# Kernel tuning notes

Measured on AMD Instinct MI355X. Metric: run time of the kernel, lower is better.

## Reference

```python
import jax, jax.numpy as jnp
import numpy as np

N_NODES = 50000
DROP_P = 0.6


def gcn_layer(x, src, dst, W, b):
    # 0P convolution: sum features of neighbors (scatter-add over edges), then linear.
    agg = jax.ops.segment_sum(x[src], dst, num_segments=N_NODES)  # [N, F]
    return agg @ W + b


def setup_inputs() -> dict:
    key = jax.random.key(0)
    k1, k2, k3, k4, k5, k6 = jax.random.split(key, 6)
    x = jax.random.normal(k1, (N_NODES, 96), dtype=jnp.float32)
    edge_index = jax.random.randint(k2, (2, 800000), 0, N_NODES, dtype=jnp.int64)
    s1 = 1.0 / np.sqrt(96.0)
    s2 = 1.0 / np.sqrt(64.0)
    W1 = jax.random.uniform(k3, (96, 64), jnp.float32, -s1, s1)
    b1 = jax.random.uniform(k4, (64,), jnp.float32, -s1, s1)
    W2 = jax.random.uniform(k5, (64, 5), jnp.float32, -s2, s2)
    b2 = jax.random.uniform(k6, (5,), jnp.float32, -s2, s2)
    return {"x": x, "edge_index": edge_index, "W1": W1, "b1": b1, "W2": W2, "b2": b2}


def reference(x, edge_index, W1, b1, W2, b2):
    src, dst = edge_index[0], edge_index[1]
    h = gcn_layer(x, src, dst, W1, b1)          # [N, hidden]
    h = jax.nn.relu(h)
    # dropout(p=0.6), deterministic mask from a fixed key
    keep = jax.random.bernoulli(jax.random.key(1), 1.0 - DROP_P, h.shape)
    h = jnp.where(keep, h / (1.0 - DROP_P), 0.0)
    out = gcn_layer(h, src, dst, W2, b2)        # [N, num_classes]
    return out
```

## Files before the change

kernel.cpp:

```cpp
#include <hip/hip_runtime.h>

#define FIN 96
#define HID 64
#define NCLS 5
#define BSH 7
#define BNODES 128
#define MAXNB 512
#define CAPSH 12
#define G1R 64
#define SXP 100

__device__ __forceinline__ unsigned rotl32(unsigned x, int d) {
    return (x << d) | (x >> (32 - d));
}

__device__ __forceinline__ void threefry2x32(unsigned k0, unsigned k1,
                                             unsigned c0, unsigned c1,
                                             unsigned& o0, unsigned& o1) {
    unsigned ks2 = k0 ^ k1 ^ 0x1BD11BDAu;
    unsigned x0 = c0 + k0, x1 = c1 + k1;
#define RND(r) { x0 += x1; x1 = rotl32(x1, r); x1 ^= x0; }
#define G0 RND(13) RND(15) RND(26) RND(6)
#define G1 RND(17) RND(29) RND(16) RND(24)
    G0; x0 += k1;  x1 += ks2 + 1u;
    G1; x0 += ks2; x1 += k0 + 2u;
    G0; x0 += k0;  x1 += k1 + 3u;
    G1; x0 += k1;  x1 += ks2 + 4u;
    G0; x0 += ks2; x1 += k0 + 5u;
#undef G0
#undef G1
#undef RND
    o0 = x0; o1 = x1;
}

__device__ __forceinline__ float drop_mask_mul(unsigned t) {
    unsigned o0, o1;
    threefry2x32(0u, 1u, 0u, t, o0, o1);
    unsigned bits = o0 ^ o1;
    float u = __uint_as_float((bits >> 9) | 0x3f800000u) - 1.0f;
    return (u < 0.4f) ? 2.5f : 0.0f;
}

__device__ __forceinline__ unsigned short f2bf(float f) {
    unsigned u = __float_as_uint(f);
    unsigned r = 0x7fffu + ((u >> 16) & 1u);
    return (unsigned short)((u + r) >> 16);
}

__device__ __forceinline__ float bflo(unsigned u) { return __uint_as_float(u << 16); }
__device__ __forceinline__ float bfhi(unsigned u) { return __uint_as_float(u & 0xffff0000u); }

__global__ __launch_bounds__(256) void gemm1_kernel(
        const float* __restrict__ x, const float* __restrict__ W,
        unsigned short* __restrict__ t1b, int* __restrict__ bktCur, int N) {
    if (blockIdx.x == 0) {
        for (int k = threadIdx.x; k < MAXNB; k += 256) bktCur[k] = k << CAPSH;
    }
    __shared__ float sX[G1R * SXP];
    __shared__ float sW[FIN * HID];
    int row0 = blockIdx.x * G1R;
    for (int i = threadIdx.x * 4; i < FIN * HID; i += 1024)
        *(float4*)&sW[i] = *(const float4*)&W[i];
    for (int i = threadIdx.x; i < G1R * (FIN / 4); i += 256) {
        int r = i / (FIN / 4), m = i % (FIN / 4);
        int gr = row0 + r;
        float4 v = make_float4(0.f, 0.f, 0.f, 0.f);
        if (gr < N) v = *(const float4*)&x[gr * FIN + m * 4];
        *(float4*)&sX[r * SXP + m * 4] = v;
    }
    __syncthreads();
    int tc = threadIdx.x & 15;
    int tr = threadIdx.x >> 4;
    float acc[4][4] = {};
    const float* xb = &sX[tr * 4 * SXP];
    for (int k = 0; k < FIN; ++k) {
        float4 w = *(const float4*)&sW[k * HID + tc * 4];
        #pragma unroll
        for (int j = 0; j < 4; ++j) {
            float xv = xb[j * SXP + k];
            acc[j][0] += xv * w.x;
            acc[j][1] += xv * w.y;
            acc[j][2] += xv * w.z;
            acc[j][3] += xv * w.w;
        }
    }
    #pragma unroll
    for (int j = 0; j < 4; ++j) {
        int gr = row0 + tr * 4 + j;
        if (gr < N) {
            ushort4 o;
            o.x = f2bf(acc[j][0]); o.y = f2bf(acc[j][1]);
            o.z = f2bf(acc[j][2]); o.w = f2bf(acc[j][3]);
            *(ushort4*)&t1b[gr * HID + tc * 4] = o;
        }
    }
}

__global__ __launch_bounds__(1024) void bin_kernel(
        const int* __restrict__ src, const int* __restrict__ dst,
        int* __restrict__ bktCur, unsigned* __restrict__ bin, int E, int NB) {
    __shared__ int hist_s[MAXNB];
    __shared__ int base_s[MAXNB];
    __shared__ int cur_s[MAXNB];
    int e0 = blockIdx.x * 4096;
    int eb = e0 + threadIdx.x * 4;
    for (int k = threadIdx.x; k < NB; k += 1024) hist_s[k] = 0;
    __syncthreads();
    int4 s4 = make_int4(0, 0, 0, 0), d4 = make_int4(-1, -1, -1, -1);
    if (eb + 3 < E) {
        s4 = *(const int4*)&src[eb];
        d4 = *(const int4*)&dst[eb];
    } else {
        int tmp[4][2];
        for (int j = 0; j < 4; ++j) {
            tmp[j][0] = (eb + j < E) ? src[eb + j] : 0;
            tmp[j][1] = (eb + j < E) ? dst[eb + j] : -1;
        }
        s4 = make_int4(tmp[0][0], tmp[1][0], tmp[2][0], tmp[3][0]);
        d4 = make_int4(tmp[0][1], tmp[1][1], tmp[2][1], tmp[3][1]);
    }
    if (d4.x >= 0) atomicAdd(&hist_s[d4.x >> BSH], 1);
    if (d4.y >= 0) atomicAdd(&hist_s[d4.y >> BSH], 1);
    if (d4.z >= 0) atomicAdd(&hist_s[d4.z >> BSH], 1);
    if (d4.w >= 0) atomicAdd(&hist_s[d4.w >> BSH], 1);
    __syncthreads();
    for (int k = threadIdx.x; k < NB; k += 1024) {
        int c = hist_s[k];
        base_s[k] = c ? atomicAdd(&bktCur[k], c) : 0;
        cur_s[k] = 0;
    }
    __syncthreads();
    int ss[4] = {s4.x, s4.y, s4.z, s4.w};
    int dd[4] = {d4.x, d4.y, d4.z, d4.w};
    #pragma unroll
    for (int j = 0; j < 4; ++j) {
        int d = dd[j];
        if (d < 0) continue;
        int k = d >> BSH;
        int slot = base_s[k] + atomicAdd(&cur_s[k], 1);
        if (slot < ((k + 1) << CAPSH))
            bin[slot] = ((unsigned)(d & (BNODES - 1)) << 16) | (unsigned)ss[j];
    }
}

__global__ __launch_bounds__(512) void sortk_kernel(
        const int* __restrict__ bktCur, const unsigned* __restrict__ bin,
        int* __restrict__ offset, int* __restrict__ count,
        unsigned short* __restrict__ sortedSrc, int N) {
    __shared__ int cnt_s[BNODES];
    __shared__ int inc_s[BNODES];
    __shared__ int cur_s[BNODES];
    int b = blockIdx.x;
    int start = b << CAPSH;
    int end = min(bktCur[b], (b + 1) << CAPSH);
    int node0 = b << BSH;
    if (threadIdx.x < BNODES) cnt_s[threadIdx.x] = 0;
    __syncthreads();
    for (int i = start + threadIdx.x; i < end; i += 512)
        atomicAdd(&cnt_s[bin[i] >> 16], 1);
    __syncthreads();
    if (threadIdx.x < BNODES)
        inc_s[threadIdx.x] = (cnt_s[threadIdx.x] + 3) & ~3;
    __syncthreads();
    #pragma unroll
    for (int off = 1; off < BNODES; off <<= 1) {
        int v = (threadIdx.x < BNODES && threadIdx.x >= off)
                ? inc_s[threadIdx.x - off] : 0;
        __syncthreads();
        if (threadIdx.x < BNODES) inc_s[threadIdx.x] += v;
        __syncthreads();
    }
    if (threadIdx.x < BNODES) {
        int pad = (cnt_s[threadIdx.x] + 3) & ~3;
        int excl = inc_s[threadIdx.x] - pad;
        cur_s[threadIdx.x] = excl;
        int node = node0 + threadIdx.x;
        if (node < N) {
            offset[node] = start + excl;
            count[node]  = cnt_s[threadIdx.x];
        }
    }
    __syncthreads();
    for (int i = start + threadIdx.x; i < end; i += 512) {
        unsigned rec = bin[i];
        int ld = (int)(rec >> 16);
        int slot = start + atomicAdd(&cur_s[ld], 1);
        if (slot < ((b + 1) << CAPSH))
            sortedSrc[slot] = (unsigned short)(rec & 0xffffu);
    }
}

__global__ __launch_bounds__(256) void agg1_fused_kernel(
        const int* __restrict__ offset, const int* __restrict__ count,
        const unsigned short* __restrict__ sortedSrc,
        const uint4* __restrict__ t1v, const float* __restrict__ b1,
        const float* __restrict__ W2, float* __restrict__ t2p, int N) {
    __shared__ float sW2[HID * NCLS];
    __shared__ float sB1[HID];
    for (int i = threadIdx.x; i < HID * NCLS; i += 256) sW2[i] = W2[i];
    if (threadIdx.x < HID) sB1[threadIdx.x] = b1[threadIdx.x];
    __syncthreads();
    int g = threadIdx.x >> 3;
    int l = threadIdx.x & 7;
    int node = blockIdx.x * 32 + g;
    if (node >= N) return;
    int beg = offset[node];
    int end = beg + count[node];
    float a0 = 0.f, a1 = 0.f, a2 = 0.f, a3 = 0.f,
          a4 = 0.f, a5 = 0.f, a6 = 0.f, a7 = 0.f;
    int i = beg;
    for (; i + 3 < end; i += 4) {
        uint2 idx = *(const uint2*)&sortedSrc[i];
        int s0 = idx.x & 0xffffu, s1 = idx.x >> 16;
        int s2 = idx.y & 0xffffu, s3 = idx.y >> 16;
        uint4 u0 = t1v[s0 * 8 + l];
        uint4 u1 = t1v[s1 * 8 + l];
        uint4 u2 = t1v[s2 * 8 + l];
        uint4 u3 = t1v[s3 * 8 + l];
        a0 += bflo(u0.x) + bflo(u1.x) + bflo(u2.x) + bflo(u3.x);
        a1 += bfhi(u0.x) + bfhi(u1.x) + bfhi(u2.x) + bfhi(u3.x);
        a2 += bflo(u0.y) + bflo(u1.y) + bflo(u2.y) + bflo(u3.y);
        a3 += bfhi(u0.y) + bfhi(u1.y) + bfhi(u2.y) + bfhi(u3.y);
        a4 += bflo(u0.z) + bflo(u1.z) + bflo(u2.z) + bflo(u3.z);
        a5 += bfhi(u0.z) + bfhi(u1.z) + bfhi(u2.z) + bfhi(u3.z);
        a6 += bflo(u0.w) + bflo(u1.w) + bflo(u2.w) + bflo(u3.w);
        a7 += bfhi(u0.w) + bfhi(u1.w) + bfhi(u2.w) + bfhi(u3.w);
    }
    for (; i < end; ++i) {
        uint4 u = t1v[(int)sortedSrc[i] * 8 + l];
        a0 += bflo(u.x); a1 += bfhi(u.x);
        a2 += bflo(u.y); a3 += bfhi(u.y);
        a4 += bflo(u.z); a5 += bfhi(u.z);
        a6 += bflo(u.w); a7 += bfhi(u.w);
    }
    int f0 = l * 8;
    unsigned tb = (unsigned)(node * HID + f0);
    float acc[8] = {a0, a1, a2, a3, a4, a5, a6, a7};
    float s0 = 0.f, s1 = 0.f, s2 = 0.f, s3 = 0.f, s4 = 0.f;
    #pragma unroll
    for (int j = 0; j < 8; ++j) {
        float h = fmaxf(acc[j] + sB1[f0 + j], 0.0f) * drop_mask_mul(tb + j);
        const float* w = &sW2[(f0 + j) * NCLS];
        s0 += h * w[0]; s1 += h * w[1]; s2 += h * w[2];
        s3 += h * w[3]; s4 += h * w[4];
    }
    #pragma unroll
    for (int off = 1; off < 8; off <<= 1) {
        s0 += __shfl_xor(s0, off);
        s1 += __shfl_xor(s1, off);
        s2 += __shfl_xor(s2, off);
        s3 += __shfl_xor(s3, off);
        s4 += __shfl_xor(s4, off);
    }
    float v = (l == 0) ? s0 : (l == 1) ? s1 : (l == 2) ? s2
             : (l == 3) ? s3 : s4;
    if (l < NCLS) t2p[node * 8 + l] = v;
}

__global__ __launch_bounds__(256) void out_fused_kernel(
        const int* __restrict__ offset, const int* __restrict__ count,
        const unsigned short* __restrict__ sortedSrc,
        const float* __restrict__ t2p, const float* __restrict__ b2,
        float* __restrict__ out, int N) {
    int tid = blockIdx.x * 256 + threadIdx.x;
    if (tid >= N * NCLS) return;
    int node = tid / NCLS;
    int c = tid - node * NCLS;
    int beg = offset[node];
    int end = beg + count[node];
    float accA = b2[c], accB = 0.f;
    int i = beg;
    for (; i + 3 < end; i += 4) {
        uint2 idx = *(const uint2*)&sortedSrc[i];
        int s0 = idx.x & 0xffffu, s1 = idx.x >> 16;
        int s2 = idx.y & 0xffffu, s3 = idx.y >> 16;
        accA += t2p[s0 * 8 + c] + t2p[s1 * 8 + c];
        accB += t2p[s2 * 8 + c] + t2p[s3 * 8 + c];
    }
    for (; i < end; ++i) accA += t2p[(int)sortedSrc[i] * 8 + c];
    out[tid] = accA + accB;
}

extern "C" void kernel_launch(void* const* d_in, const int* in_sizes, int n_in,
                              void* d_out, int out_size, void* d_ws, size_t ws_size,
                              hipStream_t stream) {
    const float* x   = (const float*)d_in[0];
    const int*   ei  = (const int*)d_in[1];
    const float* W1  = (const float*)d_in[2];
    const float* b1  = (const float*)d_in[3];
    const float* W2  = (const float*)d_in[4];
    const float* b2  = (const float*)d_in[5];
    float*       out = (float*)d_out;

    const int N = in_sizes[0] / FIN;
    const int E = in_sizes[1] / 2;
    const int* src = ei;
    const int* dst = ei + E;

    const int NB = (N + BNODES - 1) / BNODES;

    unsigned short* t1b       = (unsigned short*)d_ws;
    float*          t2p       = (float*)(t1b + (size_t)N * HID);
    int*            count     = (int*)(t2p + (size_t)N * 8);
    int*            offset    = count + N;
    int*            bktCur    = offset + N;
    unsigned*       bin       = (unsigned*)(bktCur + MAXNB);
    unsigned short* sortedSrc = (unsigned short*)(bin + ((size_t)NB << CAPSH));

    gemm1_kernel<<<(N + G1R - 1) / G1R, 256, 0, stream>>>(x, W1, t1b, bktCur, N);

    bin_kernel<<<(E + 4095) / 4096, 1024, 0, stream>>>(src, dst, bktCur, bin, E, NB);

    sortk_kernel<<<NB, 512, 0, stream>>>(bktCur, bin, offset, count, sortedSrc, N);

    agg1_fused_kernel<<<(N + 31) / 32, 256, 0, stream>>>(
        offset, count, sortedSrc, (const uint4*)t1b, b1, W2, t2p, N);

    out_fused_kernel<<<(N * NCLS + 255) / 256, 256, 0, stream>>>(
        offset, count, sortedSrc, t2p, b2, out, N);
}
```

Measured before the change: 67.94 us.

## Fuse binning into GEMM launch and merge sort with first aggregation

The edge binning now runs as extra blocks of the GEMM launch. Each block writes a per-block bucket histogram matrix and locally sorted runs, which replaces the global atomic bucket cursors. Sorting by destination and the first-layer aggregation are merged into one 1024-thread kernel per 128-node bucket, which gathers the runs into shared memory and uses a shared-memory neighbor list. This cuts the launch count from five to three and removes a pass over the sorted indices. In exchange it adds a binary search per edge, a large shared-memory footprint that lowers occupancy, and fewer blocks (one per bucket) for the aggregation step.

```diff
diff --git a/kernel.cpp b/kernel.cpp
--- a/kernel.cpp
+++ b/kernel.cpp
@@ -7,6 +7,8 @@
 #define BNODES 128
 #define MAXNB 512
 #define CAPSH 12
+#define EPB 4096
+#define MAXRUNS 256
 #define G1R 64
 #define SXP 100
 
@@ -50,167 +52,202 @@
 __device__ __forceinline__ float bflo(unsigned u) { return __uint_as_float(u << 16); }
 __device__ __forceinline__ float bfhi(unsigned u) { return __uint_as_float(u & 0xffff0000u); }
 
-__global__ __launch_bounds__(256) void gemm1_kernel(
+__global__ __launch_bounds__(256) void gemm1_bin_kernel(
         const float* __restrict__ x, const float* __restrict__ W,
-        unsigned short* __restrict__ t1b, int* __restrict__ bktCur, int N) {
-    if (blockIdx.x == 0) {
-        for (int k = threadIdx.x; k < MAXNB; k += 256) bktCur[k] = k << CAPSH;
-    }
-    __shared__ float sX[G1R * SXP];
-    __shared__ float sW[FIN * HID];
-    int row0 = blockIdx.x * G1R;
-    for (int i = threadIdx.x * 4; i < FIN * HID; i += 1024)
-        *(float4*)&sW[i] = *(const float4*)&W[i];
-    for (int i = threadIdx.x; i < G1R * (FIN / 4); i += 256) {
-        int r = i / (FIN / 4), m = i % (FIN / 4);
-        int gr = row0 + r;
-        float4 v = make_float4(0.f, 0.f, 0.f, 0.f);
-        if (gr < N) v = *(const float4*)&x[gr * FIN + m * 4];
-        *(float4*)&sX[r * SXP + m * 4] = v;
-    }
-    __syncthreads();
-    int tc = threadIdx.x & 15;
-    int tr = threadIdx.x >> 4;
-    float acc[4][4] = {};
-    const float* xb = &sX[tr * 4 * SXP];
-    for (int k = 0; k < FIN; ++k) {
-        float4 w = *(const float4*)&sW[k * HID + tc * 4];
+        unsigned short* __restrict__ t1b,
+        const int* __restrict__ src, const int* __restrict__ dst,
+        int* __restrict__ cntMat, int* __restrict__ startMat,
+        unsigned* __restrict__ bin, int N, int E, int NB, int nbb) {
+    __shared__ __align__(16) char smem[50176];
+    if ((int)blockIdx.x < nbb) {
+        int* hist_s = (int*)smem;
+        int* scan_s = hist_s + MAXNB;
+        int* cur_s  = scan_s + MAXNB;
+        int blk = blockIdx.x;
+        int e0 = blk * EPB;
+        for (int k = threadIdx.x; k < NB; k += 256) hist_s[k] = 0;
+        __syncthreads();
+        int ss[16], dd[16];
+        int base = e0 + threadIdx.x * 16;
+        #pragma unroll
+        for (int q = 0; q < 4; ++q) {
+            int b4 = base + q * 4;
+            if (b4 + 3 < E) {
+                int4 s4 = *(const int4*)&src[b4];
+                int4 d4 = *(const int4*)&dst[b4];
+                ss[q*4+0]=s4.x; ss[q*4+1]=s4.y; ss[q*4+2]=s4.z; ss[q*4+3]=s4.w;
+                dd[q*4+0]=d4.x; dd[q*4+1]=d4.y; dd[q*4+2]=d4.z; dd[q*4+3]=d4.w;
+            } else {
+                #pragma unroll
+                for (int j = 0; j < 4; ++j) {
+                    ss[q*4+j] = (b4+j < E) ? src[b4+j] : 0;
+                    dd[q*4+j] = (b4+j < E) ? dst[b4+j] : -1;
+                }
+            }
+        }
+        #pragma unroll
+        for (int j = 0; j < 16; ++j)
+            if (dd[j] >= 0) atomicAdd(&hist_s[dd[j] >> BSH], 1);
+        __syncthreads();
+        for (int k = threadIdx.x; k < NB; k += 256) scan_s[k] = hist_s[k];
+        __syncthreads();
+        for (int off = 1; off < NB; off <<= 1) {
+            int v[2]; int c = 0;
+            for (int k = threadIdx.x; k < NB; k += 256)
+                v[c++] = (k >= off) ? scan_s[k - off] : 0;
+            __syncthreads();
+            c = 0;
+            for (int k = threadIdx.x; k < NB; k += 256) scan_s[k] += v[c++];
+            __syncthreads();
+        }
+        for (int k = threadIdx.x; k < NB; k += 256) {
+            int excl = scan_s[k] - hist_s[k];
+            cntMat[k * nbb + blk]   = hist_s[k];
+            startMat[k * nbb + blk] = e0 + excl;
+            cur_s[k] = excl;
+        }
+        __syncthreads();
+        #pragma unroll
+        for (int j = 0; j < 16; ++j) {
+            int d = dd[j];
+            if (d < 0) continue;
+            int k = d >> BSH;
+            int p = e0 + atomicAdd(&cur_s[k], 1);
+            bin[p] = ((unsigned)(d & (BNODES - 1)) << 16) | (unsigned)ss[j];
+        }
+    } else {
+        float* sX = (float*)smem;
+        float* sW = (float*)(smem + 25600);
+        int row0 = ((int)blockIdx.x - nbb) * G1R;
+        for (int i = threadIdx.x * 4; i < FIN * HID; i += 1024)
+            *(float4*)&sW[i] = *(const float4*)&W[i];
+        for (int i = threadIdx.x; i < G1R * (FIN / 4); i += 256) {
+            int r = i / (FIN / 4), m = i % (FIN / 4);
+            int gr = row0 + r;
+            float4 v = make_float4(0.f, 0.f, 0.f, 0.f);
+            if (gr < N) v = *(const float4*)&x[gr * FIN + m * 4];
+            *(float4*)&sX[r * SXP + m * 4] = v;
+        }
+        __syncthreads();
+        int tc = threadIdx.x & 15;
+        int tr = threadIdx.x >> 4;
+        float acc[4][4] = {};
+        const float* xb = &sX[tr * 4 * SXP];
+        for (int k = 0; k < FIN; ++k) {
+            float4 w = *(const float4*)&sW[k * HID + tc * 4];
+            #pragma unroll
+            for (int j = 0; j < 4; ++j) {
+                float xv = xb[j * SXP + k];
+                acc[j][0] += xv * w.x;
+                acc[j][1] += xv * w.y;
+                acc[j][2] += xv * w.z;
+                acc[j][3] += xv * w.w;
+            }
+        }
         #pragma unroll
         for (int j = 0; j < 4; ++j) {
-            float xv = xb[j * SXP + k];
-            acc[j][0] += xv * w.x;
-            acc[j][1] += xv * w.y;
-            acc[j][2] += xv * w.z;
-            acc[j][3] += xv * w.w;
-        }
-    }
-    #pragma unroll
-    for (int j = 0; j < 4; ++j) {
-        int gr = row0 + tr * 4 + j;
-        if (gr < N) {
-            ushort4 o;
-            o.x = f2bf(acc[j][0]); o.y = f2bf(acc[j][1]);
-            o.z = f2bf(acc[j][2]); o.w = f2bf(acc[j][3]);
-            *(ushort4*)&t1b[gr * HID + tc * 4] = o;
-        }
-    }
-}
-
-__global__ __launch_bounds__(1024) void bin_kernel(
-        const int* __restrict__ src, const int* __restrict__ dst,
-        int* __restrict__ bktCur, unsigned* __restrict__ bin, int E, int NB) {
-    __shared__ int hist_s[MAXNB];
-    __shared__ int base_s[MAXNB];
-    __shared__ int cur_s[MAXNB];
-    int e0 = blockIdx.x * 4096;
-    int eb = e0 + threadIdx.x * 4;
-    for (int k = threadIdx.x; k < NB; k += 1024) hist_s[k] = 0;
-    __syncthreads();
-    int4 s4 = make_int4(0, 0, 0, 0), d4 = make_int4(-1, -1, -1, -1);
-    if (eb + 3 < E) {
-        s4 = *(const int4*)&src[eb];
-        d4 = *(const int4*)&dst[eb];
-    } else {
-        int tmp[4][2];
-        for (int j = 0; j < 4; ++j) {
-            tmp[j][0] = (eb + j < E) ? src[eb + j] : 0;
-            tmp[j][1] = (eb + j < E) ? dst[eb + j] : -1;
-        }
-        s4 = make_int4(tmp[0][0], tmp[1][0], tmp[2][0], tmp[3][0]);
-        d4 = make_int4(tmp[0][1], tmp[1][1], tmp[2][1], tmp[3][1]);
-    }
-    if (d4.x >= 0) atomicAdd(&hist_s[d4.x >> BSH], 1);
-    if (d4.y >= 0) atomicAdd(&hist_s[d4.y >> BSH], 1);
-    if (d4.z >= 0) atomicAdd(&hist_s[d4.z >> BSH], 1);
-    if (d4.w >= 0) atomicAdd(&hist_s[d4.w >> BSH], 1);
-    __syncthreads();
-    for (int k = threadIdx.x; k < NB; k += 1024) {
-        int c = hist_s[k];
-        base_s[k] = c ? atomicAdd(&bktCur[k], c) : 0;
-        cur_s[k] = 0;
-    }
-    __syncthreads();
-    int ss[4] = {s4.x, s4.y, s4.z, s4.w};
-    int dd[4] = {d4.x, d4.y, d4.z, d4.w};
-    #pragma unroll
-    for (int j = 0; j < 4; ++j) {
-        int d = dd[j];
-        if (d < 0) continue;
-        int k = d >> BSH;
-        int slot = base_s[k] + atomicAdd(&cur_s[k], 1);
-        if (slot < ((k + 1) << CAPSH))
-            bin[slot] = ((unsigned)(d & (BNODES - 1)) << 16) | (unsigned)ss[j];
-    }
-}
-
-__global__ __launch_bounds__(512) void sortk_kernel(
-        const int* __restrict__ bktCur, const unsigned* __restrict__ bin,
+            int gr = row0 + tr * 4 + j;
+            if (gr < N) {
+                ushort4 o;
+                o.x = f2bf(acc[j][0]); o.y = f2bf(acc[j][1]);
+                o.z = f2bf(acc[j][2]); o.w = f2bf(acc[j][3]);
+                *(ushort4*)&t1b[gr * HID + tc * 4] = o;
+            }
+        }
+    }
+}
+
+__global__ __launch_bounds__(1024) void sortagg_kernel(
+        const int* __restrict__ cntMat, const int* __restrict__ startMat,
+        const unsigned* __restrict__ bin, const uint4* __restrict__ t1v,
+        const float* __restrict__ b1, const float* __restrict__ W2,
         int* __restrict__ offset, int* __restrict__ count,
-        unsigned short* __restrict__ sortedSrc, int N) {
-    __shared__ int cnt_s[BNODES];
-    __shared__ int inc_s[BNODES];
-    __shared__ int cur_s[BNODES];
-    int b = blockIdx.x;
-    int start = b << CAPSH;
-    int end = min(bktCur[b], (b + 1) << CAPSH);
-    int node0 = b << BSH;
-    if (threadIdx.x < BNODES) cnt_s[threadIdx.x] = 0;
-    __syncthreads();
-    for (int i = start + threadIdx.x; i < end; i += 512)
-        atomicAdd(&cnt_s[bin[i] >> 16], 1);
-    __syncthreads();
-    if (threadIdx.x < BNODES)
-        inc_s[threadIdx.x] = (cnt_s[threadIdx.x] + 3) & ~3;
-    __syncthreads();
-    #pragma unroll
-    for (int off = 1; off < BNODES; off <<= 1) {
-        int v = (threadIdx.x < BNODES && threadIdx.x >= off)
-                ? inc_s[threadIdx.x - off] : 0;
-        __syncthreads();
-        if (threadIdx.x < BNODES) inc_s[threadIdx.x] += v;
-        __syncthreads();
-    }
-    if (threadIdx.x < BNODES) {
-        int pad = (cnt_s[threadIdx.x] + 3) & ~3;
-        int excl = inc_s[threadIdx.x] - pad;
-        cur_s[threadIdx.x] = excl;
-        int node = node0 + threadIdx.x;
-        if (node < N) {
-            offset[node] = start + excl;
-            count[node]  = cnt_s[threadIdx.x];
-        }
-    }
-    __syncthreads();
-    for (int i = start + threadIdx.x; i < end; i += 512) {
-        unsigned rec = bin[i];
-        int ld = (int)(rec >> 16);
-        int slot = start + atomicAdd(&cur_s[ld], 1);
-        if (slot < ((b + 1) << CAPSH))
-            sortedSrc[slot] = (unsigned short)(rec & 0xffffu);
-    }
-}
-
-__global__ __launch_bounds__(256) void agg1_fused_kernel(
-        const int* __restrict__ offset, const int* __restrict__ count,
-        const unsigned short* __restrict__ sortedSrc,
-        const uint4* __restrict__ t1v, const float* __restrict__ b1,
-        const float* __restrict__ W2, float* __restrict__ t2p, int N) {
+        unsigned short* __restrict__ sortedSrc, float* __restrict__ t2p,
+        int N, int nbb) {
+    __shared__ int cntRow[MAXRUNS];
+    __shared__ int startRow[MAXRUNS];
+    __shared__ int runOff[MAXRUNS + 1];
+    __shared__ int cnt_s[BNODES], off_s[BNODES], cur_s[BNODES];
+    __shared__ unsigned raw_s[4096];
+    __shared__ unsigned short list_s[4096];
     __shared__ float sW2[HID * NCLS];
     __shared__ float sB1[HID];
-    for (int i = threadIdx.x; i < HID * NCLS; i += 256) sW2[i] = W2[i];
-    if (threadIdx.x < HID) sB1[threadIdx.x] = b1[threadIdx.x];
-    __syncthreads();
-    int g = threadIdx.x >> 3;
-    int l = threadIdx.x & 7;
-    int node = blockIdx.x * 32 + g;
+    int b = blockIdx.x, tid = threadIdx.x;
+
+    for (int i = tid; i < HID * NCLS; i += 1024) sW2[i] = W2[i];
+    if (tid < HID) sB1[tid] = b1[tid];
+    if (tid < nbb) {
+        cntRow[tid]   = cntMat[b * nbb + tid];
+        startRow[tid] = startMat[b * nbb + tid];
+    }
+    if (tid < BNODES) cnt_s[tid] = 0;
+    if (tid == 0) runOff[0] = 0;
+    __syncthreads();
+    if (tid < nbb) runOff[1 + tid] = cntRow[tid];
+    __syncthreads();
+    for (int off = 1; off < nbb; off <<= 1) {
+        int v = 0;
+        if (tid < nbb && tid >= off) v = runOff[1 + tid - off];
+        __syncthreads();
+        if (tid < nbb) runOff[1 + tid] += v;
+        __syncthreads();
+    }
+    int T = runOff[nbb];
+    if (T > 4096) T = 4096;
+
+    for (int i = tid; i < T; i += 1024) {
+        int lo = 0, hi = nbb;
+        while (hi - lo > 1) {
+            int mid = (lo + hi) >> 1;
+            if (runOff[mid] <= i) lo = mid; else hi = mid;
+        }
+        unsigned rec = bin[startRow[lo] + (i - runOff[lo])];
+        raw_s[i] = rec;
+        atomicAdd(&cnt_s[rec >> 16], 1);
+    }
+    __syncthreads();
+    if (tid < BNODES) off_s[tid] = (cnt_s[tid] + 3) & ~3;
+    __syncthreads();
+    for (int off = 1; off < BNODES; off <<= 1) {
+        int v = 0;
+        if (tid < BNODES && tid >= off) v = off_s[tid - off];
+        __syncthreads();
+        if (tid < BNODES) off_s[tid] += v;
+        __syncthreads();
+    }
+    if (tid < BNODES) {
+        int pad  = (cnt_s[tid] + 3) & ~3;
+        int excl = off_s[tid] - pad;
+        off_s[tid] = excl;
+        cur_s[tid] = excl;
+        int node = (b << BSH) + tid;
+        if (node < N) {
+            offset[node] = (b << CAPSH) + excl;
+            count[node]  = cnt_s[tid];
+        }
+    }
+    __syncthreads();
+    for (int i = tid; i < T; i += 1024) {
+        unsigned rec = raw_s[i];
+        int ld = (int)(rec >> 16);
+        int pos = atomicAdd(&cur_s[ld], 1);
+        unsigned short sv = (unsigned short)(rec & 0xffffu);
+        if (pos < 4096) {
+            list_s[pos] = sv;
+            sortedSrc[(b << CAPSH) + pos] = sv;
+        }
+    }
+    __syncthreads();
+    int g = tid >> 3, l = tid & 7;
+    int node = (b << BSH) + g;
     if (node >= N) return;
-    int beg = offset[node];
-    int end = beg + count[node];
+    int beg = off_s[g];
+    int end = beg + cnt_s[g];
     float a0 = 0.f, a1 = 0.f, a2 = 0.f, a3 = 0.f,
           a4 = 0.f, a5 = 0.f, a6 = 0.f, a7 = 0.f;
     int i = beg;
     for (; i + 3 < end; i += 4) {
-        uint2 idx = *(const uint2*)&sortedSrc[i];
+        uint2 idx = *(const uint2*)&list_s[i];
         int s0 = idx.x & 0xffffu, s1 = idx.x >> 16;
         int s2 = idx.y & 0xffffu, s3 = idx.y >> 16;
         uint4 u0 = t1v[s0 * 8 + l];
@@ -227,7 +264,7 @@
         a7 += bfhi(u0.w) + bfhi(u1.w) + bfhi(u2.w) + bfhi(u3.w);
     }
     for (; i < end; ++i) {
-        uint4 u = t1v[(int)sortedSrc[i] * 8 + l];
+        uint4 u = t1v[(int)list_s[i] * 8 + l];
         a0 += bflo(u.x); a1 += bfhi(u.x);
         a2 += bflo(u.y); a3 += bfhi(u.y);
         a4 += bflo(u.z); a5 += bfhi(u.z);
@@ -297,24 +334,25 @@
     const int* src = ei;
     const int* dst = ei + E;
 
-    const int NB = (N + BNODES - 1) / BNODES;
+    const int NB  = (N + BNODES - 1) / BNODES;
+    const int nbb = (E + EPB - 1) / EPB;
+    const int g1b = (N + G1R - 1) / G1R;
 
     unsigned short* t1b       = (unsigned short*)d_ws;
     float*          t2p       = (float*)(t1b + (size_t)N * HID);
     int*            count     = (int*)(t2p + (size_t)N * 8);
     int*            offset    = count + N;
-    int*            bktCur    = offset + N;
-    unsigned*       bin       = (unsigned*)(bktCur + MAXNB);
-    unsigned short* sortedSrc = (unsigned short*)(bin + ((size_t)NB << CAPSH));
-
-    gemm1_kernel<<<(N + G1R - 1) / G1R, 256, 0, stream>>>(x, W1, t1b, bktCur, N);
-
-    bin_kernel<<<(E + 4095) / 4096, 1024, 0, stream>>>(src, dst, bktCur, bin, E, NB);
-
-    sortk_kernel<<<NB, 512, 0, stream>>>(bktCur, bin, offset, count, sortedSrc, N);
-
-    agg1_fused_kernel<<<(N + 31) / 32, 256, 0, stream>>>(
-        offset, count, sortedSrc, (const uint4*)t1b, b1, W2, t2p, N);
+    int*            cntMat    = offset + N;
+    int*            startMat  = cntMat + (size_t)NB * nbb;
+    unsigned*       bin       = (unsigned*)(startMat + (size_t)NB * nbb);
+    unsigned short* sortedSrc = (unsigned short*)(bin + E);
+
+    gemm1_bin_kernel<<<nbb + g1b, 256, 0, stream>>>(
+        x, W1, t1b, src, dst, cntMat, startMat, bin, N, E, NB, nbb);
+
+    sortagg_kernel<<<NB, 1024, 0, stream>>>(
+        cntMat, startMat, bin, (const uint4*)t1b, b1, W2,
+        offset, count, sortedSrc, t2p, N, nbb);
 
     out_fused_kernel<<<(N * NCLS + 255) / 256, 256, 0, stream>>>(
         offset, count, sortedSrc, t2p, b2, out, N);
```

After: 62.26 us. 1.09x faster.
